# Performance work log

Measured on AMD Instinct MI355X. Metric: run time of the kernel, lower is better.

## Reference

```python
import jax, jax.numpy as jnp
import numpy as np

N = 50000      # total batched graph nodes (both ASTs of all examples)
E = 30000      # edges per edge type
T = 8          # num edge types (no master node, no sibling edges)
H = 128        # gnn hidden = change_vector_dim // 2
TAG = 32       # change-tag embed size
CONTENT = H - TAG
VOCAB = 20000  # rows of token/content encoding table
B = 64         # num examples
STEPS = (3, 3) # layer_time_steps


def setup_inputs() -> dict:
    key = jax.random.key(0)
    ks = jax.random.split(key, 22)
    s = 0.05
    inp = {}
    inp["node_content_ids"] = jax.random.randint(ks[0], (N,), 0, VOCAB)
    inp["node_tag_ids"] = jax.random.randint(ks[1], (N,), 0, 4)
    inp["edge_src"] = jax.random.randint(ks[2], (T, E), 0, N)
    inp["edge_tgt"] = jax.random.randint(ks[3], (T, E), 0, N)
    inp["node2example"] = jnp.sort(jax.random.randint(ks[4], (N,), 0, B))
    inp["content_table"] = jax.random.normal(ks[5], (VOCAB, CONTENT)) * s
    inp["tag_embedding"] = jax.random.normal(ks[6], (4, TAG)) * s
    inp["msg_W"] = jax.random.normal(ks[7], (2, T, H, H)) * s
    inp["msg_b"] = jax.random.normal(ks[8], (2, T, H)) * s
    inp["gru0_Wih"] = jax.random.normal(ks[9], (H, 3 * H)) * s
    inp["gru0_Whh"] = jax.random.normal(ks[10], (H, 3 * H)) * s
    inp["gru0_bih"] = jax.random.normal(ks[11], (3 * H,)) * s
    inp["gru0_bhh"] = jax.random.normal(ks[12], (3 * H,)) * s
    inp["gru1_Wih"] = jax.random.normal(ks[13], (2 * H, 3 * H)) * s  # layer 1 gets residual concat -> 2H input
    inp["gru1_Whh"] = jax.random.normal(ks[14], (H, 3 * H)) * s
    inp["gru1_bih"] = jax.random.normal(ks[15], (3 * H,)) * s
    inp["gru1_bhh"] = jax.random.normal(ks[16], (3 * H,)) * s
    inp["r1_w"] = jax.random.normal(ks[17], (H,)) * s
    inp["r1_b"] = jax.random.normal(ks[18], ()) * s
    inp["r2_w"] = jax.random.normal(ks[19], (H,)) * s
    inp["r2_b"] = jax.random.normal(ks[20], ()) * s
    return inp


def _gru(x, h, Wih, Whh, bih, bhh):
    # PyTorch GRUCell gate order: r, z, n
    gi = x @ Wih + bih
    gh = h @ Whh + bhh
    i_r, i_z, i_n = jnp.split(gi, 3, axis=-1)
    h_r, h_z, h_n = jnp.split(gh, 3, axis=-1)
    r = jax.nn.sigmoid(i_r + h_r)
    z = jax.nn.sigmoid(i_z + h_z)
    n = jnp.tanh(i_n + r * h_n)
    return (1.0 - z) * n + z * h


def reference(node_content_ids, node_tag_ids, edge_src, edge_tgt, node2example,
              content_table, tag_embedding, msg_W, msg_b,
              gru0_Wih, gru0_Whh, gru0_bih, gru0_bhh,
              gru1_Wih, gru1_Whh, gru1_bih, gru1_bhh,
              r1_w, r1_b, r2_w, r2_b):
    # init node embeddings: [token/content encoding || change-tag embedding] -> [N, H]
    init = jnp.concatenate([content_table[node_content_ids],
                            tag_embedding[node_tag_ids]], axis=-1)
    states = init
    layer_out = []
    for layer, steps in enumerate(STEPS):
        for _ in range(steps):
            src_states = states[edge_src]                                   # [T,E,H] gather
            msgs = jnp.einsum('teh,thd->ted', src_states, msg_W[layer]) \
                   + msg_b[layer][:, None, :]                               # per-edge-type linear
            agg = jnp.zeros_like(states).at[edge_tgt].add(msgs)             # scatter-add to targets
            if layer == 1:
                # residual_connections={1:[0]}: concat initial states with incoming messages
                x = jnp.concatenate([init, agg], axis=-1)
                states = _gru(x, states, gru1_Wih, gru1_Whh, gru1_bih, gru1_bhh)
            else:
                states = _gru(agg, states, gru0_Wih, gru0_Whh, gru0_bih, gru0_bhh)
        layer_out.append(states)
    s1, s2 = layer_out
    # gated scalar readout per layer, pooled per example, concatenated -> [B, 2H]
    g1 = jax.nn.sigmoid(s1 @ r1_w + r1_b)[:, None]
    g2 = jax.nn.sigmoid(s2 @ r2_w + r2_b)[:, None]
    pooled1 = jax.ops.segment_sum(g1 * s1, node2example, num_segments=B)
    pooled2 = jax.ops.segment_sum(g2 * s2, node2example, num_segments=B)
    return jnp.concatenate([pooled1, pooled2], axis=-1)
```

## Files before the change

### kernel.cpp

```cpp
#include <hip/hip_runtime.h>
#include <hip/hip_bf16.h>

#define NN 50000
#define NE 30000
#define NT 8
#define HH 128
#define NB 64
#define CONT 96
#define TPB 16
#define EDGES (NT * NE)
#define SBLK 512
#define SNB ((NN + SBLK - 1) / SBLK)
#define RCH 8
#define NTILE (NN / 16)
#define NPAIR ((NTILE + 1) / 2)
#define XB ((NPAIR + 3) / 4)
#define GGRID ((((XB + 7) / 8)) * 32)

typedef __attribute__((ext_vector_type(8))) short short8;
typedef __attribute__((ext_vector_type(4))) float f32x4;

__device__ __forceinline__ float sigm(float x) { return 1.f / (1.f + __expf(-x)); }
__device__ __forceinline__ float tanhf_fast(float x) {
  float e = __expf(2.f * x);
  return 1.f - 2.f / (e + 1.f);
}
__device__ __forceinline__ unsigned short bfbits(float x) {
  __hip_bfloat16 b = __float2bfloat16(x);
  return *(unsigned short*)&b;
}

__global__ __launch_bounds__(256) void init_kernel(
    const int* __restrict__ cid, const int* __restrict__ tg,
    const float* __restrict__ ctab, const float* __restrict__ ttab,
    __hip_bfloat16* __restrict__ sbf, __hip_bfloat16* __restrict__ ibf)
{
  int i = blockIdx.x * 256 + threadIdx.x;
  if (i >= NN * HH) return;
  int n = i >> 7, d = i & 127;
  float v;
  if (d < CONT) v = ctab[(size_t)cid[n] * CONT + d];
  else          v = ttab[(size_t)tg[n] * 32 + (d - CONT)];
  __hip_bfloat16 b = __float2bfloat16(v);
  sbf[i] = b;
  ibf[i] = b;
}

__global__ __launch_bounds__(256) void hist_kernel(
    const int* __restrict__ etgt, int* __restrict__ cnt)
{
  int i = blockIdx.x * 256 + threadIdx.x;
  if (i >= EDGES) return;
  atomicAdd(&cnt[etgt[i]], 1);
}

__global__ __launch_bounds__(SBLK) void scanA_kernel(
    const int* __restrict__ cnt, int* __restrict__ row_ptr, int* __restrict__ bsum)
{
  __shared__ int sm[SBLK];
  const int tid = threadIdx.x;
  const int i = blockIdx.x * SBLK + tid;
  int v = (i < NN) ? cnt[i] : 0;
  sm[tid] = v;
  __syncthreads();
  for (int off = 1; off < SBLK; off <<= 1) {
    int t = (tid >= off) ? sm[tid - off] : 0;
    __syncthreads();
    sm[tid] += t;
    __syncthreads();
  }
  if (i < NN) row_ptr[i] = sm[tid] - v;
  if (tid == SBLK - 1) bsum[blockIdx.x] = sm[tid];
}

__global__ __launch_bounds__(128) void scanB_kernel(
    const int* __restrict__ bsum, int* __restrict__ boff, int* __restrict__ row_ptr)
{
  __shared__ int sm[128];
  const int tid = threadIdx.x;
  int v = (tid < SNB) ? bsum[tid] : 0;
  sm[tid] = v;
  __syncthreads();
  for (int off = 1; off < 128; off <<= 1) {
    int t = (tid >= off) ? sm[tid - off] : 0;
    __syncthreads();
    sm[tid] += t;
    __syncthreads();
  }
  if (tid < SNB) boff[tid] = sm[tid] - v;
  if (tid == 127) row_ptr[NN] = sm[127];
}

__global__ __launch_bounds__(SBLK) void scanC_kernel(
    int* __restrict__ row_ptr, int* __restrict__ cnt2, const int* __restrict__ boff)
{
  int i = blockIdx.x * SBLK + threadIdx.x;
  if (i >= NN) return;
  int r = row_ptr[i] + boff[blockIdx.x];
  row_ptr[i] = r;
  cnt2[i] = r;
}

__global__ __launch_bounds__(256) void scatter_kernel(
    const int* __restrict__ etgt, int* __restrict__ cnt2, int* __restrict__ perm)
{
  int i = blockIdx.x * 256 + threadIdx.x;
  if (i >= EDGES) return;
  perm[i] = atomicAdd(&cnt2[etgt[i]], 1);
}

__global__ __launch_bounds__(128) void exbound_kernel(
    const int* __restrict__ n2e, int* __restrict__ ebnd)
{
  int ex = threadIdx.x;
  if (ex > NB) return;
  int lo = 0, hi = NN;
  while (lo < hi) { int mid = (lo + hi) >> 1; if (n2e[mid] < ex) lo = mid + 1; else hi = mid; }
  ebnd[ex] = lo;
}

__device__ __forceinline__ void gru_swz_one(
    const float* __restrict__ W, __hip_bfloat16* __restrict__ out, int KSL, int mode, int i)
{
  int j = i & 7, lane = (i >> 3) & 63, kk = (i >> 9) % KSL, nt = i / (KSL * 512);
  int hi = lane >> 4, lo = lane & 15;
  int p = kk * 32 + hi * 8 + j;
  int k;
  if (mode == 0)      k = p;
  else if (mode == 1) k = (p & 7) * 16 + (p >> 3);
  else                k = (p < 128) ? p : 128 + ((p - 128) & 7) * 16 + ((p - 128) >> 3);
  out[i] = __float2bfloat16(W[(size_t)k * 384 + nt * 16 + lo]);
}

__global__ __launch_bounds__(256) void wswz_all_kernel(
    const float* __restrict__ msgW, __hip_bfloat16* __restrict__ wswz,
    const float* __restrict__ g0Wih, __hip_bfloat16* __restrict__ w0ih,
    const float* __restrict__ g0Whh, __hip_bfloat16* __restrict__ w0hh,
    const float* __restrict__ g1Wih, __hip_bfloat16* __restrict__ w1ih,
    const float* __restrict__ g1Whh, __hip_bfloat16* __restrict__ w1hh)
{
  int i = blockIdx.x * 256 + threadIdx.x;
  if (i < 262144) {
    int j = i & 7, lane = (i >> 3) & 63, kk = (i >> 9) & 3, nt = (i >> 11) & 7, lt = i >> 14;
    int hi = lane >> 4, lo = lane & 15;
    int k = kk * 32 + hi * 8 + j;
    wswz[i] = __float2bfloat16(msgW[((size_t)lt * HH + k) * HH + nt * 16 + lo]);
    return;
  }
  i -= 262144;
  if (i < 49152)  { gru_swz_one(g0Wih, w0ih, 4, 1, i); return; }
  i -= 49152;
  if (i < 49152)  { gru_swz_one(g0Whh, w0hh, 4, 0, i); return; }
  i -= 49152;
  if (i < 98304)  { gru_swz_one(g1Wih, w1ih, 8, 2, i); return; }
  i -= 98304;
  if (i < 49152)  { gru_swz_one(g1Whh, w1hh, 4, 0, i); return; }
}

__global__ __launch_bounds__(256) void msg_mfma_kernel(
    const __hip_bfloat16* __restrict__ sbf, const int* __restrict__ esrc,
    const int* __restrict__ perm, const __hip_bfloat16* __restrict__ wswz,
    const float* __restrict__ ball, __hip_bfloat16* __restrict__ msgs, int layer)
{
  __shared__ short8 Wl[8 * 4 * 64];
  const int t = blockIdx.y;
  {
    const float4* wg = (const float4*)(wswz + (size_t)(layer * NT + t) * 16384);
    float4* wl = (float4*)Wl;
    for (int i = threadIdx.x; i < 2048; i += 256) wl[i] = wg[i];
  }
  const int lane = threadIdx.x & 63;
  const int wv   = threadIdx.x >> 6;
  const int hi = lane >> 4, lo = lane & 15;
  float bias_v[8];
#pragma unroll
  for (int nt = 0; nt < 8; ++nt)
    bias_v[nt] = ball[(layer * NT + t) * HH + nt * 16 + lo];
  __syncthreads();

  const int tile_end = min((int)(blockIdx.x + 1) * TPB, NE / 16);
  for (int tile = blockIdx.x * TPB + wv; tile < tile_end; tile += 4) {
    const int e0 = tile * 16;
    const int src = esrc[t * NE + e0 + lo];
    const short* srow = (const short*)(sbf + (size_t)src * HH);
    short8 a[4];
#pragma unroll
    for (int kk = 0; kk < 4; ++kk)
      a[kk] = *(const short8*)(srow + kk * 32 + hi * 8);
    int slot[4];
#pragma unroll
    for (int r = 0; r < 4; ++r) slot[r] = perm[t * NE + e0 + hi * 4 + r];
    f32x4 acc[8];
#pragma unroll
    for (int nt = 0; nt < 8; ++nt) acc[nt] = (f32x4){0.f, 0.f, 0.f, 0.f};
#pragma unroll
    for (int nt = 0; nt < 8; ++nt)
#pragma unroll
      for (int kk = 0; kk < 4; ++kk)
        acc[nt] = __builtin_amdgcn_mfma_f32_16x16x32_bf16(
            a[kk], Wl[(nt * 4 + kk) * 64 + lane], acc[nt], 0, 0, 0);
#pragma unroll
    for (int r = 0; r < 4; ++r) {
      short8 m;
#pragma unroll
      for (int nt = 0; nt < 8; ++nt)
        ((unsigned short*)&m)[nt] = bfbits(acc[nt][r] + bias_v[nt]);
      *(short8*)((short*)msgs + (size_t)slot[r] * HH + lo * 8) = m;
    }
  }
}

__global__ __launch_bounds__(256) void reduce_kernel(
    const __hip_bfloat16* __restrict__ msgs, const int* __restrict__ row_ptr,
    __hip_bfloat16* __restrict__ agg)
{
  const int lane = threadIdx.x & 63;
  const int n = blockIdx.x * 4 + (threadIdx.x >> 6);
  if (n >= NN) return;
  const int b = row_ptr[n], e = row_ptr[n + 1];
  float a0 = 0.f, a1 = 0.f;
  for (int i = b; i < e; ++i) {
    unsigned int v = *(const unsigned int*)((const short*)msgs + (size_t)i * HH + lane * 2);
    a0 += __uint_as_float(v << 16);
    a1 += __uint_as_float(v & 0xffff0000u);
  }
  unsigned int o = ((unsigned int)bfbits(a1) << 16) | bfbits(a0);
  *(unsigned int*)((short*)agg + (size_t)n * HH + lane * 2) = o;
}

template <int KSL>
__global__ __launch_bounds__(256) void gru_mfma_kernel(
    const __hip_bfloat16* __restrict__ agg,
    const __hip_bfloat16* __restrict__ ibf,
    const __hip_bfloat16* __restrict__ hbf,
    const __hip_bfloat16* __restrict__ Wih_s,
    const __hip_bfloat16* __restrict__ Whh_s,
    const float* __restrict__ bih, const float* __restrict__ bhh,
    __hip_bfloat16* __restrict__ sbf_out)
{
  const int wg = blockIdx.x;
  const int xb = (wg >> 5) * 8 + (wg & 7);
  const int dtg = (wg >> 3) & 3;
  if (xb >= XB) return;

  __shared__ short8 BihL[2 * 3 * KSL * 64];
  {
    const short8* Bih_g = (const short8*)Wih_s;
    for (int i = threadIdx.x; i < 2 * 3 * KSL * 64; i += 256) {
      int lane_i = i & 63, kk = (i >> 6) % KSL, g = ((i >> 6) / KSL) % 3, d2 = (i >> 6) / (KSL * 3);
      BihL[i] = Bih_g[((size_t)(dtg * 2 + d2 + 8 * g) * KSL + kk) * 64 + lane_i];
    }
  }
  const int lane = threadIdx.x & 63;
  const int wv   = threadIdx.x >> 6;
  const int hi = lane >> 4, lo = lane & 15;
  float birv[2], bizv[2], binv[2], bhrv[2], bhzv[2], bhnv[2];
#pragma unroll
  for (int d2 = 0; d2 < 2; ++d2) {
    const int c = (dtg * 2 + d2) * 16 + lo;
    birv[d2] = bih[c]; bizv[d2] = bih[c + 128]; binv[d2] = bih[c + 256];
    bhrv[d2] = bhh[c]; bhzv[d2] = bhh[c + 128]; bhnv[d2] = bhh[c + 256];
  }
  __syncthreads();

  const int pt = xb * 4 + wv;
  if (pt >= NPAIR) return;
  const int t0 = pt * 2;
  const bool two = (t0 + 1 < NTILE);

  short8 ax[2][KSL], ah[2][4];
#pragma unroll
  for (int u = 0; u < 2; ++u) {
    const int nb = ((u && two) ? t0 + 1 : t0) * 16;
    const short* arow = (const short*)(agg + (size_t)(nb + lo) * HH);
    const short* hrow = (const short*)(hbf + (size_t)(nb + lo) * HH);
    if (KSL == 8) {
      const short* irow = (const short*)(ibf + (size_t)(nb + lo) * HH);
#pragma unroll
      for (int kk = 0; kk < 4; ++kk) {
        ax[u][kk]     = *(const short8*)(irow + kk * 32 + hi * 8);
        ax[u][kk + 4] = *(const short8*)(arow + kk * 32 + hi * 8);
      }
    } else {
#pragma unroll
      for (int kk = 0; kk < KSL; ++kk)
        ax[u][kk] = *(const short8*)(arow + kk * 32 + hi * 8);
    }
#pragma unroll
    for (int kk = 0; kk < 4; ++kk)
      ah[u][kk] = *(const short8*)(hrow + kk * 32 + hi * 8);
  }

  const short8* __restrict__ Bhh_g = (const short8*)Whh_s;

  f32x4 aR[2][2], aZ[2][2], aNi[2][2], aNh[2][2];
#pragma unroll
  for (int d2 = 0; d2 < 2; ++d2)
#pragma unroll
    for (int u = 0; u < 2; ++u) {
      aR[d2][u] = (f32x4){0.f, 0.f, 0.f, 0.f};
      aZ[d2][u] = (f32x4){0.f, 0.f, 0.f, 0.f};
      aNi[d2][u] = (f32x4){0.f, 0.f, 0.f, 0.f};
      aNh[d2][u] = (f32x4){0.f, 0.f, 0.f, 0.f};
    }

#pragma unroll
  for (int d2 = 0; d2 < 2; ++d2) {
#pragma unroll
    for (int kk = 0; kk < KSL; ++kk) {
      short8 br = BihL[((d2 * 3 + 0) * KSL + kk) * 64 + lane];
      short8 bz = BihL[((d2 * 3 + 1) * KSL + kk) * 64 + lane];
      short8 bn = BihL[((d2 * 3 + 2) * KSL + kk) * 64 + lane];
#pragma unroll
      for (int u = 0; u < 2; ++u) {
        aR[d2][u]  = __builtin_amdgcn_mfma_f32_16x16x32_bf16(ax[u][kk], br, aR[d2][u], 0, 0, 0);
        aZ[d2][u]  = __builtin_amdgcn_mfma_f32_16x16x32_bf16(ax[u][kk], bz, aZ[d2][u], 0, 0, 0);
        aNi[d2][u] = __builtin_amdgcn_mfma_f32_16x16x32_bf16(ax[u][kk], bn, aNi[d2][u], 0, 0, 0);
      }
    }
#pragma unroll
    for (int kk = 0; kk < 4; ++kk) {
      const int dt = dtg * 2 + d2;
      short8 br = Bhh_g[((size_t)(dt     ) * 4 + kk) * 64 + lane];
      short8 bz = Bhh_g[((size_t)(dt +  8) * 4 + kk) * 64 + lane];
      short8 bn = Bhh_g[((size_t)(dt + 16) * 4 + kk) * 64 + lane];
#pragma unroll
      for (int u = 0; u < 2; ++u) {
        aR[d2][u]  = __builtin_amdgcn_mfma_f32_16x16x32_bf16(ah[u][kk], br, aR[d2][u], 0, 0, 0);
        aZ[d2][u]  = __builtin_amdgcn_mfma_f32_16x16x32_bf16(ah[u][kk], bz, aZ[d2][u], 0, 0, 0);
        aNh[d2][u] = __builtin_amdgcn_mfma_f32_16x16x32_bf16(ah[u][kk], bn, aNh[d2][u], 0, 0, 0);
      }
    }
  }

  const int uend = two ? 2 : 1;
  for (int u = 0; u < uend; ++u) {
    const int nb = (t0 + u) * 16;
#pragma unroll
    for (int d2 = 0; d2 < 2; ++d2) {
      const int c = (dtg * 2 + d2) * 16 + lo;
#pragma unroll
      for (int r = 0; r < 4; ++r) {
        const int node = nb + hi * 4 + r;
        const float rg = sigm(aR[d2][u][r] + birv[d2] + bhrv[d2]);
        const float zg = sigm(aZ[d2][u][r] + bizv[d2] + bhzv[d2]);
        const float ng = tanhf_fast(aNi[d2][u][r] + binv[d2] + rg * (aNh[d2][u][r] + bhnv[d2]));
        const float hc = __bfloat162float(hbf[(size_t)node * HH + c]);
        sbf_out[(size_t)node * HH + c] = __float2bfloat16((1.f - zg) * ng + zg * hc);
      }
    }
  }
}

__global__ __launch_bounds__(256) void readout_kernel(
    const __hip_bfloat16* __restrict__ sbf, const int* __restrict__ ebnd,
    const float* __restrict__ rw, const float* __restrict__ rb,
    float* __restrict__ out, int coff)
{
  __shared__ float sm[4][128];
  const int ex = blockIdx.x / RCH, ch = blockIdx.x % RCH;
  const int s = ebnd[ex], e = ebnd[ex + 1];
  const int lane = threadIdx.x & 63;
  const int wv   = threadIdx.x >> 6;
  const float w0 = rw[2 * lane], w1 = rw[2 * lane + 1], rbv = rb[0];
  float a0 = 0.f, a1 = 0.f;
  for (int n = s + ch * 4 + wv; n < e; n += 4 * RCH) {
    unsigned int v = *(const unsigned int*)((const short*)sbf + (size_t)n * HH + lane * 2);
    const float s0 = __uint_as_float(v << 16);
    const float s1 = __uint_as_float(v & 0xffff0000u);
    float p = s0 * w0 + s1 * w1;
#pragma unroll
    for (int o = 32; o; o >>= 1) p += __shfl_xor(p, o, 64);
    const float g = sigm(p + rbv);
    a0 += g * s0;
    a1 += g * s1;
  }
  sm[wv][2 * lane] = a0;
  sm[wv][2 * lane + 1] = a1;
  __syncthreads();
  if (wv == 0) {
    const int c0 = 2 * lane, c1 = 2 * lane + 1;
    float v0 = sm[0][c0] + sm[1][c0] + sm[2][c0] + sm[3][c0];
    float v1 = sm[0][c1] + sm[1][c1] + sm[2][c1] + sm[3][c1];
    atomicAdd(&out[(size_t)ex * (2 * HH) + coff + c0], v0);
    atomicAdd(&out[(size_t)ex * (2 * HH) + coff + c1], v1);
  }
}

extern "C" void kernel_launch(void* const* d_in, const int* in_sizes, int n_in,
                              void* d_out, int out_size, void* d_ws, size_t ws_size,
                              hipStream_t stream)
{
  const int*   cid   = (const int*)d_in[0];
  const int*   tg    = (const int*)d_in[1];
  const int*   esrc  = (const int*)d_in[2];
  const int*   etgt  = (const int*)d_in[3];
  const int*   n2e   = (const int*)d_in[4];
  const float* ctab  = (const float*)d_in[5];
  const float* ttab  = (const float*)d_in[6];
  const float* msgW  = (const float*)d_in[7];
  const float* msgb  = (const float*)d_in[8];
  const float* g0Wih = (const float*)d_in[9];
  const float* g0Whh = (const float*)d_in[10];
  const float* g0bih = (const float*)d_in[11];
  const float* g0bhh = (const float*)d_in[12];
  const float* g1Wih = (const float*)d_in[13];
  const float* g1Whh = (const float*)d_in[14];
  const float* g1bih = (const float*)d_in[15];
  const float* g1bhh = (const float*)d_in[16];
  const float* r1w   = (const float*)d_in[17];
  const float* r1b   = (const float*)d_in[18];
  const float* r2w   = (const float*)d_in[19];
  const float* r2b   = (const float*)d_in[20];

  float* out = (float*)d_out;
  __hip_bfloat16* sb0  = (__hip_bfloat16*)d_ws;
  __hip_bfloat16* sb1  = sb0 + (size_t)NN * HH;
  __hip_bfloat16* ibf  = sb1 + (size_t)NN * HH;
  __hip_bfloat16* agg  = ibf + (size_t)NN * HH;
  __hip_bfloat16* msgs = agg + (size_t)NN * HH;
  __hip_bfloat16* wswz = msgs + (size_t)EDGES * HH;
  __hip_bfloat16* w0ih = wswz + 262144;
  __hip_bfloat16* w0hh = w0ih + 24 * 4 * 512;
  __hip_bfloat16* w1ih = w0hh + 24 * 4 * 512;
  __hip_bfloat16* w1hh = w1ih + 24 * 8 * 512;
  int* row_ptr = (int*)(w1hh + 24 * 4 * 512);
  int* cnt     = row_ptr + NN + 1;
  int* cnt2    = cnt + NN;
  int* perm    = cnt2 + NN;
  int* bsum    = perm + EDGES;
  int* boff    = bsum + SNB;
  int* ebnd    = boff + SNB;

  hipMemsetAsync(d_out, 0, (size_t)NB * 2 * HH * sizeof(float), stream);
  hipMemsetAsync(cnt, 0, (size_t)NN * sizeof(int), stream);
  const int eblocks = (EDGES + 255) / 256;
  hist_kernel<<<eblocks, 256, 0, stream>>>(etgt, cnt);
  scanA_kernel<<<SNB, SBLK, 0, stream>>>(cnt, row_ptr, bsum);
  scanB_kernel<<<1, 128, 0, stream>>>(bsum, boff, row_ptr);
  scanC_kernel<<<SNB, SBLK, 0, stream>>>(row_ptr, cnt2, boff);
  scatter_kernel<<<eblocks, 256, 0, stream>>>(etgt, cnt2, perm);
  exbound_kernel<<<1, 128, 0, stream>>>(n2e, ebnd);

  wswz_all_kernel<<<507904 / 256, 256, 0, stream>>>(msgW, wswz, g0Wih, w0ih, g0Whh, w0hh,
                                                    g1Wih, w1ih, g1Whh, w1hh);
  init_kernel<<<(NN * HH + 255) / 256, 256, 0, stream>>>(cid, tg, ctab, ttab, sb0, ibf);

  dim3 mgrid((NE / 16 + TPB - 1) / TPB, NT);
  const int rblocks = (NN + 3) / 4;
  __hip_bfloat16* cur = sb0;
  __hip_bfloat16* nxt = sb1;
  for (int s = 0; s < 3; ++s) {
    msg_mfma_kernel<<<mgrid, 256, 0, stream>>>(cur, esrc, perm, wswz, msgb, msgs, 0);
    reduce_kernel<<<rblocks, 256, 0, stream>>>(msgs, row_ptr, agg);
    gru_mfma_kernel<4><<<GGRID, 256, 0, stream>>>(agg, ibf, cur, w0ih, w0hh,
                                                  g0bih, g0bhh, nxt);
    __hip_bfloat16* t = cur; cur = nxt; nxt = t;
  }
  readout_kernel<<<NB * RCH, 256, 0, stream>>>(cur, ebnd, r1w, r1b, out, 0);

  for (int s = 0; s < 3; ++s) {
    msg_mfma_kernel<<<mgrid, 256, 0, stream>>>(cur, esrc, perm, wswz, msgb, msgs, 1);
    reduce_kernel<<<rblocks, 256, 0, stream>>>(msgs, row_ptr, agg);
    gru_mfma_kernel<8><<<GGRID, 256, 0, stream>>>(agg, ibf, cur, w1ih, w1hh,
                                                  g1bih, g1bhh, nxt);
    __hip_bfloat16* t = cur; cur = nxt; nxt = t;
  }
  readout_kernel<<<NB * RCH, 256, 0, stream>>>(cur, ebnd, r2w, r2b, out, HH);
}
```

Baseline: 591.2 us.

## Make GRU kernel persistent with wider per-block output slices

The GRU kernel becomes a persistent kernel with a fixed grid of 768 blocks. Each block loops over node-pair tiles and covers a templated number of output column tiles per block: 4 of the 8 for layer 0, 2 for layer 1. This amortises the LDS staging of the input weights across many tiles and loads each node's activations once for more output columns, at the cost of more LDS per block and possibly lower occupancy. Separately, the example-boundary binary search is folded into scanB_kernel, which removes one launch.

```diff
diff --git a/kernel.cpp b/kernel.cpp
--- a/kernel.cpp
+++ b/kernel.cpp
@@ -15,7 +15,7 @@
 #define NTILE (NN / 16)
 #define NPAIR ((NTILE + 1) / 2)
 #define XB ((NPAIR + 3) / 4)
-#define GGRID ((((XB + 7) / 8)) * 32)
+#define GPERS 768
 
 typedef __attribute__((ext_vector_type(8))) short short8;
 typedef __attribute__((ext_vector_type(4))) float f32x4;
@@ -74,7 +74,8 @@
 }
 
 __global__ __launch_bounds__(128) void scanB_kernel(
-    const int* __restrict__ bsum, int* __restrict__ boff, int* __restrict__ row_ptr)
+    const int* __restrict__ bsum, int* __restrict__ boff, int* __restrict__ row_ptr,
+    const int* __restrict__ n2e, int* __restrict__ ebnd)
 {
   __shared__ int sm[128];
   const int tid = threadIdx.x;
@@ -89,6 +90,11 @@
   }
   if (tid < SNB) boff[tid] = sm[tid] - v;
   if (tid == 127) row_ptr[NN] = sm[127];
+  if (tid <= NB) {
+    int lo = 0, hi = NN;
+    while (lo < hi) { int mid = (lo + hi) >> 1; if (n2e[mid] < tid) lo = mid + 1; else hi = mid; }
+    ebnd[tid] = lo;
+  }
 }
 
 __global__ __launch_bounds__(SBLK) void scanC_kernel(
@@ -107,16 +113,6 @@
   int i = blockIdx.x * 256 + threadIdx.x;
   if (i >= EDGES) return;
   perm[i] = atomicAdd(&cnt2[etgt[i]], 1);
-}
-
-__global__ __launch_bounds__(128) void exbound_kernel(
-    const int* __restrict__ n2e, int* __restrict__ ebnd)
-{
-  int ex = threadIdx.x;
-  if (ex > NB) return;
-  int lo = 0, hi = NN;
-  while (lo < hi) { int mid = (lo + hi) >> 1; if (n2e[mid] < ex) lo = mid + 1; else hi = mid; }
-  ebnd[ex] = lo;
 }
 
 __device__ __forceinline__ void gru_swz_one(
@@ -228,7 +224,7 @@
   *(unsigned int*)((short*)agg + (size_t)n * HH + lane * 2) = o;
 }
 
-template <int KSL>
+template <int KSL, int DTG>
 __global__ __launch_bounds__(256) void gru_mfma_kernel(
     const __hip_bfloat16* __restrict__ agg,
     const __hip_bfloat16* __restrict__ ibf,
@@ -238,115 +234,112 @@
     const float* __restrict__ bih, const float* __restrict__ bhh,
     __hip_bfloat16* __restrict__ sbf_out)
 {
-  const int wg = blockIdx.x;
-  const int xb = (wg >> 5) * 8 + (wg & 7);
-  const int dtg = (wg >> 3) & 3;
-  if (xb >= XB) return;
-
-  __shared__ short8 BihL[2 * 3 * KSL * 64];
+  constexpr int D2 = 8 / DTG;
+  constexpr int NSLOT = GPERS / (8 * DTG);
+  const int b = blockIdx.x;
+  const int xcd = b & 7;
+  const int dtg = (b >> 3) & (DTG - 1);
+  const int slot = b / (8 * DTG);
+
+  __shared__ short8 BihL[D2 * 3 * KSL * 64];
   {
     const short8* Bih_g = (const short8*)Wih_s;
-    for (int i = threadIdx.x; i < 2 * 3 * KSL * 64; i += 256) {
+    for (int i = threadIdx.x; i < D2 * 3 * KSL * 64; i += 256) {
       int lane_i = i & 63, kk = (i >> 6) % KSL, g = ((i >> 6) / KSL) % 3, d2 = (i >> 6) / (KSL * 3);
-      BihL[i] = Bih_g[((size_t)(dtg * 2 + d2 + 8 * g) * KSL + kk) * 64 + lane_i];
+      BihL[i] = Bih_g[((size_t)(dtg * D2 + d2 + 8 * g) * KSL + kk) * 64 + lane_i];
     }
   }
   const int lane = threadIdx.x & 63;
   const int wv   = threadIdx.x >> 6;
   const int hi = lane >> 4, lo = lane & 15;
-  float birv[2], bizv[2], binv[2], bhrv[2], bhzv[2], bhnv[2];
-#pragma unroll
-  for (int d2 = 0; d2 < 2; ++d2) {
-    const int c = (dtg * 2 + d2) * 16 + lo;
+  float birv[D2], bizv[D2], binv[D2], bhrv[D2], bhzv[D2], bhnv[D2];
+#pragma unroll
+  for (int d2 = 0; d2 < D2; ++d2) {
+    const int c = (dtg * D2 + d2) * 16 + lo;
     birv[d2] = bih[c]; bizv[d2] = bih[c + 128]; binv[d2] = bih[c + 256];
     bhrv[d2] = bhh[c]; bhzv[d2] = bhh[c + 128]; bhnv[d2] = bhh[c + 256];
   }
   __syncthreads();
 
-  const int pt = xb * 4 + wv;
-  if (pt >= NPAIR) return;
-  const int t0 = pt * 2;
-  const bool two = (t0 + 1 < NTILE);
-
-  short8 ax[2][KSL], ah[2][4];
-#pragma unroll
-  for (int u = 0; u < 2; ++u) {
-    const int nb = ((u && two) ? t0 + 1 : t0) * 16;
-    const short* arow = (const short*)(agg + (size_t)(nb + lo) * HH);
-    const short* hrow = (const short*)(hbf + (size_t)(nb + lo) * HH);
-    if (KSL == 8) {
-      const short* irow = (const short*)(ibf + (size_t)(nb + lo) * HH);
+  const short8* __restrict__ Bhh_g = (const short8*)Whh_s;
+
+  for (int xb = xcd + 8 * slot; xb < XB; xb += 8 * NSLOT) {
+    const int pt = xb * 4 + wv;
+    if (pt >= NPAIR) continue;
+    const int t0 = pt * 2;
+    const bool two = (t0 + 1 < NTILE);
+
+    short8 ax[2][KSL], ah[2][4];
+#pragma unroll
+    for (int u = 0; u < 2; ++u) {
+      const int nb = ((u && two) ? t0 + 1 : t0) * 16;
+      const short* arow = (const short*)(agg + (size_t)(nb + lo) * HH);
+      const short* hrow = (const short*)(hbf + (size_t)(nb + lo) * HH);
+      if (KSL == 8) {
+        const short* irow = (const short*)(ibf + (size_t)(nb + lo) * HH);
+#pragma unroll
+        for (int kk = 0; kk < 4; ++kk) {
+          ax[u][kk]     = *(const short8*)(irow + kk * 32 + hi * 8);
+          ax[u][kk + 4] = *(const short8*)(arow + kk * 32 + hi * 8);
+        }
+      } else {
+#pragma unroll
+        for (int kk = 0; kk < KSL; ++kk)
+          ax[u][kk] = *(const short8*)(arow + kk * 32 + hi * 8);
+      }
+#pragma unroll
+      for (int kk = 0; kk < 4; ++kk)
+        ah[u][kk] = *(const short8*)(hrow + kk * 32 + hi * 8);
+    }
+
+#pragma unroll
+    for (int d2 = 0; d2 < D2; ++d2) {
+      const int dt = dtg * D2 + d2;
+      f32x4 aR[2], aZ[2], aNi[2], aNh[2];
+#pragma unroll
+      for (int u = 0; u < 2; ++u) {
+        aR[u] = (f32x4){0.f, 0.f, 0.f, 0.f};
+        aZ[u] = (f32x4){0.f, 0.f, 0.f, 0.f};
+        aNi[u] = (f32x4){0.f, 0.f, 0.f, 0.f};
+        aNh[u] = (f32x4){0.f, 0.f, 0.f, 0.f};
+      }
+#pragma unroll
+      for (int kk = 0; kk < KSL; ++kk) {
+        short8 br = BihL[((d2 * 3 + 0) * KSL + kk) * 64 + lane];
+        short8 bz = BihL[((d2 * 3 + 1) * KSL + kk) * 64 + lane];
+        short8 bn = BihL[((d2 * 3 + 2) * KSL + kk) * 64 + lane];
+#pragma unroll
+        for (int u = 0; u < 2; ++u) {
+          aR[u]  = __builtin_amdgcn_mfma_f32_16x16x32_bf16(ax[u][kk], br, aR[u], 0, 0, 0);
+          aZ[u]  = __builtin_amdgcn_mfma_f32_16x16x32_bf16(ax[u][kk], bz, aZ[u], 0, 0, 0);
+          aNi[u] = __builtin_amdgcn_mfma_f32_16x16x32_bf16(ax[u][kk], bn, aNi[u], 0, 0, 0);
+        }
+      }
 #pragma unroll
       for (int kk = 0; kk < 4; ++kk) {
-        ax[u][kk]     = *(const short8*)(irow + kk * 32 + hi * 8);
-        ax[u][kk + 4] = *(const short8*)(arow + kk * 32 + hi * 8);
+        short8 br = Bhh_g[((size_t)(dt     ) * 4 + kk) * 64 + lane];
+        short8 bz = Bhh_g[((size_t)(dt +  8) * 4 + kk) * 64 + lane];
+        short8 bn = Bhh_g[((size_t)(dt + 16) * 4 + kk) * 64 + lane];
+#pragma unroll
+        for (int u = 0; u < 2; ++u) {
+          aR[u]  = __builtin_amdgcn_mfma_f32_16x16x32_bf16(ah[u][kk], br, aR[u], 0, 0, 0);
+          aZ[u]  = __builtin_amdgcn_mfma_f32_16x16x32_bf16(ah[u][kk], bz, aZ[u], 0, 0, 0);
+          aNh[u] = __builtin_amdgcn_mfma_f32_16x16x32_bf16(ah[u][kk], bn, aNh[u], 0, 0, 0);
+        }
       }
-    } else {
-#pragma unroll
-      for (int kk = 0; kk < KSL; ++kk)
-        ax[u][kk] = *(const short8*)(arow + kk * 32 + hi * 8);
-    }
-#pragma unroll
-    for (int kk = 0; kk < 4; ++kk)
-      ah[u][kk] = *(const short8*)(hrow + kk * 32 + hi * 8);
-  }
-
-  const short8* __restrict__ Bhh_g = (const short8*)Whh_s;
-
-  f32x4 aR[2][2], aZ[2][2], aNi[2][2], aNh[2][2];
-#pragma unroll
-  for (int d2 = 0; d2 < 2; ++d2)
-#pragma unroll
-    for (int u = 0; u < 2; ++u) {
-      aR[d2][u] = (f32x4){0.f, 0.f, 0.f, 0.f};
-      aZ[d2][u] = (f32x4){0.f, 0.f, 0.f, 0.f};
-      aNi[d2][u] = (f32x4){0.f, 0.f, 0.f, 0.f};
-      aNh[d2][u] = (f32x4){0.f, 0.f, 0.f, 0.f};
-    }
-
-#pragma unroll
-  for (int d2 = 0; d2 < 2; ++d2) {
-#pragma unroll
-    for (int kk = 0; kk < KSL; ++kk) {
-      short8 br = BihL[((d2 * 3 + 0) * KSL + kk) * 64 + lane];
-      short8 bz = BihL[((d2 * 3 + 1) * KSL + kk) * 64 + lane];
-      short8 bn = BihL[((d2 * 3 + 2) * KSL + kk) * 64 + lane];
-#pragma unroll
-      for (int u = 0; u < 2; ++u) {
-        aR[d2][u]  = __builtin_amdgcn_mfma_f32_16x16x32_bf16(ax[u][kk], br, aR[d2][u], 0, 0, 0);
-        aZ[d2][u]  = __builtin_amdgcn_mfma_f32_16x16x32_bf16(ax[u][kk], bz, aZ[d2][u], 0, 0, 0);
-        aNi[d2][u] = __builtin_amdgcn_mfma_f32_16x16x32_bf16(ax[u][kk], bn, aNi[d2][u], 0, 0, 0);
-      }
-    }
-#pragma unroll
-    for (int kk = 0; kk < 4; ++kk) {
-      const int dt = dtg * 2 + d2;
-      short8 br = Bhh_g[((size_t)(dt     ) * 4 + kk) * 64 + lane];
-      short8 bz = Bhh_g[((size_t)(dt +  8) * 4 + kk) * 64 + lane];
-      short8 bn = Bhh_g[((size_t)(dt + 16) * 4 + kk) * 64 + lane];
-#pragma unroll
-      for (int u = 0; u < 2; ++u) {
-        aR[d2][u]  = __builtin_amdgcn_mfma_f32_16x16x32_bf16(ah[u][kk], br, aR[d2][u], 0, 0, 0);
-        aZ[d2][u]  = __builtin_amdgcn_mfma_f32_16x16x32_bf16(ah[u][kk], bz, aZ[d2][u], 0, 0, 0);
-        aNh[d2][u] = __builtin_amdgcn_mfma_f32_16x16x32_bf16(ah[u][kk], bn, aNh[d2][u], 0, 0, 0);
-      }
-    }
-  }
-
-  const int uend = two ? 2 : 1;
-  for (int u = 0; u < uend; ++u) {
-    const int nb = (t0 + u) * 16;
-#pragma unroll
-    for (int d2 = 0; d2 < 2; ++d2) {
-      const int c = (dtg * 2 + d2) * 16 + lo;
-#pragma unroll
-      for (int r = 0; r < 4; ++r) {
-        const int node = nb + hi * 4 + r;
-        const float rg = sigm(aR[d2][u][r] + birv[d2] + bhrv[d2]);
-        const float zg = sigm(aZ[d2][u][r] + bizv[d2] + bhzv[d2]);
-        const float ng = tanhf_fast(aNi[d2][u][r] + binv[d2] + rg * (aNh[d2][u][r] + bhnv[d2]));
-        const float hc = __bfloat162float(hbf[(size_t)node * HH + c]);
-        sbf_out[(size_t)node * HH + c] = __float2bfloat16((1.f - zg) * ng + zg * hc);
+      const int c = dt * 16 + lo;
+      const int uend = two ? 2 : 1;
+      for (int u = 0; u < uend; ++u) {
+        const int nb = (t0 + u) * 16;
+#pragma unroll
+        for (int r = 0; r < 4; ++r) {
+          const int node = nb + hi * 4 + r;
+          const float rg = sigm(aR[u][r] + birv[d2] + bhrv[d2]);
+          const float zg = sigm(aZ[u][r] + bizv[d2] + bhzv[d2]);
+          const float ng = tanhf_fast(aNi[u][r] + binv[d2] + rg * (aNh[u][r] + bhnv[d2]));
+          const float hc = __bfloat162float(hbf[(size_t)node * HH + c]);
+          sbf_out[(size_t)node * HH + c] = __float2bfloat16((1.f - zg) * ng + zg * hc);
+        }
       }
     }
   }
@@ -437,10 +430,9 @@
   const int eblocks = (EDGES + 255) / 256;
   hist_kernel<<<eblocks, 256, 0, stream>>>(etgt, cnt);
   scanA_kernel<<<SNB, SBLK, 0, stream>>>(cnt, row_ptr, bsum);
-  scanB_kernel<<<1, 128, 0, stream>>>(bsum, boff, row_ptr);
+  scanB_kernel<<<1, 128, 0, stream>>>(bsum, boff, row_ptr, n2e, ebnd);
   scanC_kernel<<<SNB, SBLK, 0, stream>>>(row_ptr, cnt2, boff);
   scatter_kernel<<<eblocks, 256, 0, stream>>>(etgt, cnt2, perm);
-  exbound_kernel<<<1, 128, 0, stream>>>(n2e, ebnd);
 
   wswz_all_kernel<<<507904 / 256, 256, 0, stream>>>(msgW, wswz, g0Wih, w0ih, g0Whh, w0hh,
                                                     g1Wih, w1ih, g1Whh, w1hh);
@@ -453,8 +445,8 @@
   for (int s = 0; s < 3; ++s) {
     msg_mfma_kernel<<<mgrid, 256, 0, stream>>>(cur, esrc, perm, wswz, msgb, msgs, 0);
     reduce_kernel<<<rblocks, 256, 0, stream>>>(msgs, row_ptr, agg);
-    gru_mfma_kernel<4><<<GGRID, 256, 0, stream>>>(agg, ibf, cur, w0ih, w0hh,
-                                                  g0bih, g0bhh, nxt);
+    gru_mfma_kernel<4, 2><<<GPERS, 256, 0, stream>>>(agg, ibf, cur, w0ih, w0hh,
+                                                     g0bih, g0bhh, nxt);
     __hip_bfloat16* t = cur; cur = nxt; nxt = t;
   }
   readout_kernel<<<NB * RCH, 256, 0, stream>>>(cur, ebnd, r1w, r1b, out, 0);
@@ -462,8 +454,8 @@
   for (int s = 0; s < 3; ++s) {
     msg_mfma_kernel<<<mgrid, 256, 0, stream>>>(cur, esrc, perm, wswz, msgb, msgs, 1);
     reduce_kernel<<<rblocks, 256, 0, stream>>>(msgs, row_ptr, agg);
-    gru_mfma_kernel<8><<<GGRID, 256, 0, stream>>>(agg, ibf, cur, w1ih, w1hh,
-                                                  g1bih, g1bhh, nxt);
+    gru_mfma_kernel<8, 4><<<GPERS, 256, 0, stream>>>(agg, ibf, cur, w1ih, w1hh,
+                                                     g1bih, g1bhh, nxt);
     __hip_bfloat16* t = cur; cur = nxt; nxt = t;
   }
   readout_kernel<<<NB * RCH, 256, 0, stream>>>(cur, ebnd, r2w, r2b, out, HH);
```

Measured after the change: 647.1 us. 9.5% more time.
